# Optimization experiments

Hardware: AMD Instinct MI355X
Metric: run time of the kernel (lower is better)

Reference implementation:

```python
import jax, jax.numpy as jnp
import numpy as np

APP_DIM = 27
FEA_PE = 6
VIEW_PE = 6
FEATURE_C = 128
DENSITY_SHIFT = -10.0
DISTANCE_SCALE = 25.0
IN_MLPC = 2 * VIEW_PE * 3 + 2 * FEA_PE * APP_DIM + 3 + APP_DIM  # 390


def positional_encoding(x, freqs):
    # x: [..., C] -> [..., 2*freqs*C]
    freq_bands = (2.0 ** jnp.arange(freqs)).astype(x.dtype)
    pts = (x[..., None] * freq_bands).reshape(x.shape[:-1] + (freqs * x.shape[-1],))
    return jnp.concatenate([jnp.sin(pts), jnp.cos(pts)], axis=-1)


def alpha2weights(alpha):
    # alpha: [N_rays, N_samples]; last sample forced opaque (as in source)
    alpha = alpha.at[:, -1].set(1.0)
    trans = jnp.concatenate(
        [jnp.ones((alpha.shape[0], 1), alpha.dtype), 1.0 - alpha + 1e-10], axis=-1)
    T = jnp.cumprod(trans, axis=-1)
    weights = alpha * T[:, :-1]
    return weights, T


def setup_inputs() -> dict:
    key = jax.random.key(0)
    ks = jax.random.split(key, 12)
    N_rays, N_samples = 4096, 128
    sigma_feat = jax.random.normal(ks[0], (N_rays, N_samples), jnp.float32)
    app_features = 0.1 * jax.random.normal(ks[1], (N_rays, N_samples, APP_DIM), jnp.float32)
    vd = jax.random.normal(ks[2], (N_rays, N_samples, 3), jnp.float32)
    viewdirs = vd / (jnp.linalg.norm(vd, axis=-1, keepdims=True) + 1e-8)
    dists = 0.02 * jax.random.uniform(ks[3], (N_rays, N_samples), jnp.float32)

    def linear(k, fan_in, fan_out):
        kw, kb = jax.random.split(k)
        lim = 1.0 / np.sqrt(fan_in)
        W = jax.random.uniform(kw, (fan_in, fan_out), jnp.float32, -lim, lim)
        b = jax.random.uniform(kb, (fan_out,), jnp.float32, -lim, lim)
        return W, b

    W1, b1 = linear(ks[4], IN_MLPC, FEATURE_C)
    W2, b2 = linear(ks[5], FEATURE_C, FEATURE_C)
    W3, _ = linear(ks[6], FEATURE_C, 3)
    b3 = jnp.zeros((3,), jnp.float32)  # bias of last layer initialized to 0 in source
    return {"sigma_feat": sigma_feat, "app_features": app_features,
            "viewdirs": viewdirs, "dists": dists,
            "W1": W1, "b1": b1, "W2": W2, "b2": b2, "W3": W3, "b3": b3}


def reference(sigma_feat, app_features, viewdirs, dists, W1, b1, W2, b2, W3, b3):
    # feature2density: softplus with density_shift
    sigma = jax.nn.softplus(sigma_feat + DENSITY_SHIFT)
    alpha = 1.0 - jnp.exp(-sigma * dists * DISTANCE_SCALE)  # [N_rays, N_samples]
    weights, _T = alpha2weights(alpha)

    # MLPRender_Fea: cat[features, viewdirs, PE(features), PE(viewdirs)]
    mlp_in = jnp.concatenate(
        [app_features, viewdirs,
         positional_encoding(app_features, FEA_PE),
         positional_encoding(viewdirs, VIEW_PE)], axis=-1)  # [R, S, 390]
    h = jax.nn.relu(jnp.einsum('rsc,cf->rsf', mlp_in, W1) + b1)
    h = jax.nn.relu(jnp.einsum('rsf,fg->rsg', h, W2) + b2)
    rgb = jax.nn.sigmoid(jnp.einsum('rsg,go->rso', h, W3) + b3)  # [R, S, 3]

    rgb_map = jnp.sum(weights[..., None] * rgb, axis=-2)  # [R, 3]
    return rgb_map
```

## Files before the change

kernel.cpp:

```cpp
#include <hip/hip_runtime.h>
#include <math.h>

typedef unsigned short u16;
using bf16x8 = __attribute__((ext_vector_type(8))) short;
using f32x4  = __attribute__((ext_vector_type(4))) float;

#define NS      128
#define NBLOCKS 4096
#define NSLICE  19

#define POOLSZ 32768
#define OH2    16384

#define BAR() do { asm volatile("s_waitcnt lgkmcnt(0)" ::: "memory");        \
                   __builtin_amdgcn_s_barrier();                              \
                   asm volatile("" ::: "memory"); } while (0)

#define MF(A,B,C) __builtin_amdgcn_mfma_f32_16x16x32_bf16((A),(B),(C),0,0,0)

__device__ __forceinline__ u16 f2bf(float f) {
    unsigned int i = __float_as_uint(f);
    return (u16)((i + 0x7FFFu + ((i >> 16) & 1u)) >> 16);
}

__device__ __forceinline__ unsigned pk(float hi, float lo) {
    unsigned r;
    asm("v_cvt_pk_bf16_f32 %0, %1, %2" : "=v"(r) : "v"(lo), "v"(hi));
    return r;
}
__device__ __forceinline__ u16 f2bf1(float f) {
    return (u16)((__float_as_uint(f) + 0x8000u) >> 16);
}

__device__ __forceinline__ int afoff_h(int m, int k) {
    int chunk = ((k >> 5) * 8 + (m >> 4)) * 64 + ((k >> 3) & 3) * 16 + (m & 15);
    chunk ^= (k >> 3) & 3;
    return chunk * 8 + (k & 7);
}

__device__ __forceinline__ int orig_k(int ch, int slot) {
    if (ch < 27) {
        if (slot == 0) return ch;
        if (slot <= 6) return 30 + ch * 6 + (slot - 1);
        return 192 + ch * 6 + (slot - 7);
    } else {
        int c = ch - 27;
        if (slot == 0) return 27 + c;
        if (slot <= 6) return 354 + c * 6 + (slot - 1);
        return 372 + c * 6 + (slot - 7);
    }
}

__device__ __forceinline__ float ldch(const float* ap, const float* vp, int c) {
    return (c < 27) ? ap[c] : vp[c - 27];
}

__device__ __forceinline__ void build_x(u16* dst, float v) {
    float rev = v * 0.15915494309189535f;
    rev -= floorf(rev);
    float s0 = __builtin_amdgcn_sinf(rev);
    float c0 = __builtin_amdgcn_cosf(rev);
    float s1 = 2.f * s0 * c0, c1 = c0 * c0 - s0 * s0;
    float s2 = 2.f * s1 * c1, c2 = c1 * c1 - s1 * s1;
    float s3 = 2.f * s2 * c2, c3 = c2 * c2 - s2 * s2;
    float s4 = 2.f * s3 * c3, c4 = c3 * c3 - s3 * s3;
    float s5 = 2.f * s4 * c4, c5 = c4 * c4 - s4 * s4;
    uint4 lo, hi;
    lo.x = pk(s0, v);  lo.y = pk(s2, s1);  lo.z = pk(s4, s3);  lo.w = pk(c0, s5);
    hi.x = pk(c2, c1); hi.y = pk(c4, c3);  hi.z = pk(0.f, c5); hi.w = 0u;
    *(uint4*)(dst)       = lo;
    *(uint4*)(dst + 128) = hi;
}

__global__ __launch_bounds__(256) void prep_kernel(
    const float* __restrict__ W1, const float* __restrict__ W2,
    const float* __restrict__ W3, u16* __restrict__ ws)
{
    int idx = blockIdx.x * 256 + threadIdx.x;
    if (idx < 61440) {
        int j = idx & 7, lane = (idx >> 3) & 63, nt = (idx >> 9) & 7, ks = idx >> 12;
        int q = lane >> 4, l15 = lane & 15;
        int klocal = q * 8 + j;
        int ch = ks * 2 + (klocal >> 4);
        int slot = klocal & 15;
        int n = nt * 16 + l15;
        ws[idx] = (slot < 13) ? f2bf(W1[orig_k(ch, slot) * 128 + n]) : (u16)0;
    } else if (idx < 77824) {
        int i2 = idx - 61440;
        int j = i2 & 7, lane = (i2 >> 3) & 63, nt = (i2 >> 9) & 7, ks = i2 >> 12;
        int k = ks * 32 + (lane >> 4) * 8 + j;
        int n = nt * 16 + (lane & 15);
        ws[idx] = f2bf(W2[k * 128 + n]);
    } else if (idx < 79872) {
        int i3 = idx - 77824;
        int j = i3 & 7, lane = (i3 >> 3) & 63, ks = i3 >> 9;
        int k = ks * 32 + (lane >> 4) * 8 + j;
        int n = lane & 15;
        ws[idx] = (n < 3) ? f2bf(W3[k * 3 + n]) : (u16)0;
    }
}

#define LOADB2(N0, N1, s)                                                     \
    if ((s) < NSLICE) {                                                       \
        const u16* wp = wp0 + (s) * 4096;                                     \
        N0 = *(const bf16x8*)(wp);                                            \
        N1 = *(const bf16x8*)(wp + 512);                                      \
    }

#define BODYX(s, C0,C1, N0,N1)                                                \
  {                                                                           \
    LOADB2(N0, N1, (s)+2);                                                    \
    const u16* ab = pool + ((s)&7)*4096 + (wm*256 + lane)*8;                  \
    bf16x8 a0 = *(const bf16x8*)(ab);                                         \
    bf16x8 a1 = *(const bf16x8*)(ab + 512);                                   \
    __builtin_amdgcn_s_setprio(1);                                            \
    acc[0][0]=MF(a0,C0,acc[0][0]); acc[0][1]=MF(a0,C1,acc[0][1]);             \
    acc[1][0]=MF(a1,C0,acc[1][0]); acc[1][1]=MF(a1,C1,acc[1][1]);             \
    a0 = *(const bf16x8*)(ab + 1024);                                         \
    a1 = *(const bf16x8*)(ab + 1536);                                         \
    acc[2][0]=MF(a0,C0,acc[2][0]); acc[2][1]=MF(a0,C1,acc[2][1]);             \
    acc[3][0]=MF(a1,C0,acc[3][0]); acc[3][1]=MF(a1,C1,acc[3][1]);             \
    __builtin_amdgcn_s_setprio(0);                                            \
  }

#define BODYH(s, C0,C1, N0,N1)                                                \
  {                                                                           \
    LOADB2(N0, N1, (s)+2);                                                    \
    int cb = ((((s)-15)*512) + wm*256 + lane) ^ quad;                         \
    bf16x8 a0 = *(const bf16x8*)(pool + cb*8);                                \
    bf16x8 a1 = *(const bf16x8*)(pool + (cb+64)*8);                           \
    __builtin_amdgcn_s_setprio(1);                                            \
    acc[0][0]=MF(a0,C0,acc[0][0]); acc[0][1]=MF(a0,C1,acc[0][1]);             \
    acc[1][0]=MF(a1,C0,acc[1][0]); acc[1][1]=MF(a1,C1,acc[1][1]);             \
    a0 = *(const bf16x8*)(pool + (cb+128)*8);                                 \
    a1 = *(const bf16x8*)(pool + (cb+192)*8);                                 \
    acc[2][0]=MF(a0,C0,acc[2][0]); acc[2][1]=MF(a0,C1,acc[2][1]);             \
    acc[3][0]=MF(a1,C0,acc[3][0]); acc[3][1]=MF(a1,C1,acc[3][1]);             \
    __builtin_amdgcn_s_setprio(0);                                            \
  }

#define GENDQ(p)                                                              \
  {                                                                           \
    if (8*(p)+8  + cl < 30)                                                   \
        build_x(pool + ((2*(p)+2)&3)*8192 + (cl>>1)*4096 + bxoff, pv_a);      \
    if (8*(p)+12 + cl < 30)                                                   \
        build_x(pool + ((2*(p)+3)&3)*8192 + (cl>>1)*4096 + bxoff, pv_b);      \
    pv_a = pv_c; pv_b = pv_d;                                                 \
    if (8*(p)+24 + cl < 30) pv_c = ldch(ap, vp, 8*(p)+24 + cl);               \
    if (8*(p)+28 + cl < 30) pv_d = ldch(ap, vp, 8*(p)+28 + cl);               \
    BAR();                                                                    \
  }

__global__ __launch_bounds__(512, 4) void render_kernel(
    const float* __restrict__ sigma_g, const float* __restrict__ app_g,
    const float* __restrict__ view_g,  const float* __restrict__ dists_g,
    const float* __restrict__ b1_g,    const float* __restrict__ b2_g,
    const float* __restrict__ b3_g,    const u16* __restrict__ ws,
    float* __restrict__ out_g)
{
    __shared__ __align__(16) u16 pool[POOLSZ];
    __shared__ __align__(16) float part[NS * 3];
    __shared__ float scanS;
    __shared__ float sum2[6];

    const int tid  = threadIdx.x;
    const int lane = tid & 63;
    const int wave = tid >> 6;
    const int l15  = lane & 15;
    const int quad = lane >> 4;
    const int wm   = wave >> 2;
    const int wn   = wave & 3;

    const int r  = blockIdx.x;
    const int rb = r * NS;
    const int row = tid & 127;
    const int cl  = tid >> 7;
    const float* ap = app_g  + (rb + row) * 27;
    const float* vp = view_g + (rb + row) * 3;
    const int bxoff = (row >> 4) * 512 + (((cl & 1) * 32) + (row & 15)) * 8;

    const u16* wp0 = ws + (wn * 128 + lane) * 8;
    bf16x8 bP0, bP1, bQ0, bQ1, bR0, bR1;
    LOADB2(bP0, bP1, 0);
    LOADB2(bQ0, bQ1, 1);

    float pv_a = ldch(ap, vp, cl);
    float pv_b = ldch(ap, vp, 4 + cl);
    float pv_c = ldch(ap, vp, 8 + cl);
    float pv_d = ldch(ap, vp, 12 + cl);

    float alpha = 0.f, prod = 1.f, wr = 0.f;
    if (tid < NS) {
        float x  = sigma_g[rb + tid] - 10.f;
        float sp = (x > 20.f) ? x : log1pf(expf(x));
        alpha = 1.f - expf(-sp * dists_g[rb + tid] * 25.f);
        if (tid == NS - 1) alpha = 1.f;
        float tb = 1.f - alpha + 1e-10f;
        prod = tb;
        #pragma unroll
        for (int d = 1; d < 64; d <<= 1) {
            float v = __shfl_up(prod, d);
            if (lane >= d) prod *= v;
        }
        if (tid == 63) scanS = prod;
    }

    build_x(pool +        (cl >> 1) * 4096 + bxoff, pv_a);
    build_x(pool + 8192 + (cl >> 1) * 4096 + bxoff, pv_b);
    pv_a = pv_c; pv_b = pv_d;
    pv_c = ldch(ap, vp, 16 + cl);
    pv_d = ldch(ap, vp, 20 + cl);
    BAR();

    if (tid < NS) {
        float prev = __shfl_up(prod, 1);
        float base = (lane == 0) ? 1.f : prev;
        float scale = (wave == 1) ? scanS : 1.f;
        wr = alpha * base * scale;
    }

    const f32x4 vzero = {0.f, 0.f, 0.f, 0.f};
    f32x4 acc[4][2];
    #pragma unroll
    for (int mt = 0; mt < 4; ++mt)
        #pragma unroll
        for (int nt = 0; nt < 2; ++nt) acc[mt][nt] = vzero;

    BODYX(0,  bP0,bP1, bR0,bR1);
    BODYX(1,  bQ0,bQ1, bP0,bP1);
    BODYX(2,  bR0,bR1, bQ0,bQ1);
    BODYX(3,  bP0,bP1, bR0,bR1);  GENDQ(0);
    BODYX(4,  bQ0,bQ1, bP0,bP1);
    BODYX(5,  bR0,bR1, bQ0,bQ1);
    BODYX(6,  bP0,bP1, bR0,bR1);
    BODYX(7,  bQ0,bQ1, bP0,bP1);  GENDQ(1);
    BODYX(8,  bR0,bR1, bQ0,bQ1);
    BODYX(9,  bP0,bP1, bR0,bR1);
    BODYX(10, bQ0,bQ1, bP0,bP1);
    BODYX(11, bR0,bR1, bQ0,bQ1);  GENDQ(2);
    const float b1r0 = b1_g[wn * 32 + l15];
    const float b1r1 = b1_g[wn * 32 + 16 + l15];
    BODYX(12, bP0,bP1, bR0,bR1);
    BODYX(13, bQ0,bQ1, bP0,bP1);
    BODYX(14, bR0,bR1, bQ0,bQ1);

    #pragma unroll
    for (int mt = 0; mt < 4; ++mt)
        #pragma unroll
        for (int nt = 0; nt < 2; ++nt) {
            int col = wn * 32 + nt * 16 + l15;
            #pragma unroll
            for (int rr = 0; rr < 4; ++rr) {
                int rw = wm * 64 + mt * 16 + quad * 4 + rr;
                pool[afoff_h(rw, col)] =
                    f2bf1(fmaxf(acc[mt][nt][rr] + ((nt == 0) ? b1r0 : b1r1), 0.f));
            }
            acc[mt][nt] = vzero;
        }
    BAR();

    const float b2r0 = b2_g[wn * 32 + l15];
    const float b2r1 = b2_g[wn * 32 + 16 + l15];

    BODYH(15, bP0,bP1, bR0,bR1);
    BODYH(16, bQ0,bQ1, bP0,bP1);
    BODYH(17, bR0,bR1, bQ0,bQ1);
    BODYH(18, bP0,bP1, bR0,bR1);

    #pragma unroll
    for (int mt = 0; mt < 4; ++mt)
        #pragma unroll
        for (int nt = 0; nt < 2; ++nt) {
            int col = wn * 32 + nt * 16 + l15;
            #pragma unroll
            for (int rr = 0; rr < 4; ++rr) {
                int rw = wm * 64 + mt * 16 + quad * 4 + rr;
                pool[OH2 + afoff_h(rw, col)] =
                    f2bf1(fmaxf(acc[mt][nt][rr] + ((nt == 0) ? b2r0 : b2r1), 0.f));
            }
        }
    BAR();

    const u16* w3r = ws + 77824;
    const float b3v = (l15 < 3) ? b3_g[l15] : 0.f;
    f32x4 acc3 = vzero;
    #pragma unroll
    for (int ks = 0; ks < 4; ++ks) {
        bf16x8 w3f = *(const bf16x8*)(w3r + (ks * 64 + lane) * 8);
        int c = ((ks * 8 + wave) * 64 + lane) ^ quad;
        bf16x8 a3 = *(const bf16x8*)(pool + OH2 + c * 8);
        acc3 = MF(a3, w3f, acc3);
    }
    if (l15 < 3) {
        #pragma unroll
        for (int rr = 0; rr < 4; ++rr) {
            int rw = wave * 16 + quad * 4 + rr;
            float v = acc3[rr] + b3v;
            part[rw * 3 + l15] = 1.f / (1.f + expf(-v));
        }
    }
    BAR();

    if (tid < NS) {
        float v0 = wr * part[tid * 3 + 0];
        float v1 = wr * part[tid * 3 + 1];
        float v2 = wr * part[tid * 3 + 2];
        #pragma unroll
        for (int d = 1; d < 64; d <<= 1) {
            v0 += __shfl_xor(v0, d);
            v1 += __shfl_xor(v1, d);
            v2 += __shfl_xor(v2, d);
        }
        if (lane == 0) {
            sum2[wave * 3 + 0] = v0;
            sum2[wave * 3 + 1] = v1;
            sum2[wave * 3 + 2] = v2;
        }
    }
    BAR();
    if (tid == 0) {
        out_g[r * 3 + 0] = sum2[0] + sum2[3];
        out_g[r * 3 + 1] = sum2[1] + sum2[4];
        out_g[r * 3 + 2] = sum2[2] + sum2[5];
    }
}

extern "C" void kernel_launch(void* const* d_in, const int* in_sizes, int n_in,
                              void* d_out, int out_size, void* d_ws, size_t ws_size,
                              hipStream_t stream) {
    (void)in_sizes; (void)n_in; (void)out_size; (void)ws_size;
    const float* sigma = (const float*)d_in[0];
    const float* app   = (const float*)d_in[1];
    const float* view  = (const float*)d_in[2];
    const float* dists = (const float*)d_in[3];
    const float* W1    = (const float*)d_in[4];
    const float* b1    = (const float*)d_in[5];
    const float* W2    = (const float*)d_in[6];
    const float* b2    = (const float*)d_in[7];
    const float* W3    = (const float*)d_in[8];
    const float* b3    = (const float*)d_in[9];
    float* out = (float*)d_out;

    u16* ws = (u16*)d_ws;

    prep_kernel<<<312, 256, 0, stream>>>(W1, W2, W3, ws);
    render_kernel<<<NBLOCKS, 512, 0, stream>>>(sigma, app, view, dists,
                                               b1, b2, b3, ws, out);
}
```

Before: 193.2 us.

## Pack layer-1 K dimension densely by frequency to cut padded MFMA slices

Changes the first-layer K layout from 16 slots per channel (13 used, 3 zero pads) to grouping one frequency term per 32-wide K slice across 30 channels, so layer 1 runs 13 K-slices instead of 15. Each thread now owns 8 channels and produces successive sin/cos terms by repeated angle doubling, writing one slice pair per step into a ring of LDS buffers. The hidden-layer buffers are relocated into the same ring to match. This removes padded MFMA work and reshuffles positional-encoding generation, at the cost of more registers per thread and a different barrier schedule.

Result: no change. 195.1 us (+1.0%).

```diff
diff --git a/kernel.cpp b/kernel.cpp
--- a/kernel.cpp
+++ b/kernel.cpp
@@ -7,10 +7,9 @@
 
 #define NS      128
 #define NBLOCKS 4096
-#define NSLICE  19
+#define NSLICE  17
 
 #define POOLSZ 32768
-#define OH2    16384
 
 #define BAR() do { asm volatile("s_waitcnt lgkmcnt(0)" ::: "memory");        \
                    __builtin_amdgcn_s_barrier();                              \
@@ -32,10 +31,15 @@
     return (u16)((__float_as_uint(f) + 0x8000u) >> 16);
 }
 
-__device__ __forceinline__ int afoff_h(int m, int k) {
-    int chunk = ((k >> 5) * 8 + (m >> 4)) * 64 + ((k >> 3) & 3) * 16 + (m & 15);
-    chunk ^= (k >> 3) & 3;
-    return chunk * 8 + (k & 7);
+__device__ __forceinline__ int afoff_h1(int m, int k) {
+    int e = (k >> 3) & 3;
+    int chunk = (m >> 4) * 64 + e * 16 + (m & 15);
+    return ((5 + (k >> 5)) & 7) * 4096 + (chunk ^ e) * 8 + (k & 7);
+}
+__device__ __forceinline__ int afoff_h2(int m, int k) {
+    int e = (k >> 3) & 3;
+    int chunk = (m >> 4) * 64 + e * 16 + (m & 15);
+    return ((1 + (k >> 5)) & 7) * 4096 + (chunk ^ e) * 8 + (k & 7);
 }
 
 __device__ __forceinline__ int orig_k(int ch, int slot) {
@@ -51,25 +55,9 @@
     }
 }
 
-__device__ __forceinline__ float ldch(const float* ap, const float* vp, int c) {
-    return (c < 27) ? ap[c] : vp[c - 27];
-}
-
-__device__ __forceinline__ void build_x(u16* dst, float v) {
-    float rev = v * 0.15915494309189535f;
-    rev -= floorf(rev);
-    float s0 = __builtin_amdgcn_sinf(rev);
-    float c0 = __builtin_amdgcn_cosf(rev);
-    float s1 = 2.f * s0 * c0, c1 = c0 * c0 - s0 * s0;
-    float s2 = 2.f * s1 * c1, c2 = c1 * c1 - s1 * s1;
-    float s3 = 2.f * s2 * c2, c3 = c2 * c2 - s2 * s2;
-    float s4 = 2.f * s3 * c3, c4 = c3 * c3 - s3 * s3;
-    float s5 = 2.f * s4 * c4, c5 = c4 * c4 - s4 * s4;
-    uint4 lo, hi;
-    lo.x = pk(s0, v);  lo.y = pk(s2, s1);  lo.z = pk(s4, s3);  lo.w = pk(c0, s5);
-    hi.x = pk(c2, c1); hi.y = pk(c4, c3);  hi.z = pk(0.f, c5); hi.w = 0u;
-    *(uint4*)(dst)       = lo;
-    *(uint4*)(dst + 128) = hi;
+__device__ __forceinline__ int cons_slot(int j) {
+    if (j == 0) return 0;
+    return (j & 1) ? (j + 1) / 2 : 6 + j / 2;
 }
 
 __global__ __launch_bounds__(256) void prep_kernel(
@@ -77,24 +65,22 @@
     const float* __restrict__ W3, u16* __restrict__ ws)
 {
     int idx = blockIdx.x * 256 + threadIdx.x;
-    if (idx < 61440) {
-        int j = idx & 7, lane = (idx >> 3) & 63, nt = (idx >> 9) & 7, ks = idx >> 12;
+    if (idx < 53248) {
+        int jj = idx & 7, lane = (idx >> 3) & 63, nt = (idx >> 9) & 7, j = idx >> 12;
         int q = lane >> 4, l15 = lane & 15;
-        int klocal = q * 8 + j;
-        int ch = ks * 2 + (klocal >> 4);
-        int slot = klocal & 15;
+        int ch = q * 8 + jj;
         int n = nt * 16 + l15;
-        ws[idx] = (slot < 13) ? f2bf(W1[orig_k(ch, slot) * 128 + n]) : (u16)0;
-    } else if (idx < 77824) {
-        int i2 = idx - 61440;
-        int j = i2 & 7, lane = (i2 >> 3) & 63, nt = (i2 >> 9) & 7, ks = i2 >> 12;
-        int k = ks * 32 + (lane >> 4) * 8 + j;
+        ws[idx] = (ch < 30) ? f2bf(W1[orig_k(ch, cons_slot(j)) * 128 + n]) : (u16)0;
+    } else if (idx < 69632) {
+        int i2 = idx - 53248;
+        int jj = i2 & 7, lane = (i2 >> 3) & 63, nt = (i2 >> 9) & 7, ks = i2 >> 12;
+        int k = ks * 32 + (lane >> 4) * 8 + jj;
         int n = nt * 16 + (lane & 15);
         ws[idx] = f2bf(W2[k * 128 + n]);
-    } else if (idx < 79872) {
-        int i3 = idx - 77824;
-        int j = i3 & 7, lane = (i3 >> 3) & 63, ks = i3 >> 9;
-        int k = ks * 32 + (lane >> 4) * 8 + j;
+    } else if (idx < 71680) {
+        int i3 = idx - 69632;
+        int jj = i3 & 7, lane = (i3 >> 3) & 63, ks = i3 >> 9;
+        int k = ks * 32 + (lane >> 4) * 8 + jj;
         int n = lane & 15;
         ws[idx] = (n < 3) ? f2bf(W3[k * 3 + n]) : (u16)0;
     }
@@ -126,7 +112,7 @@
 #define BODYH(s, C0,C1, N0,N1)                                                \
   {                                                                           \
     LOADB2(N0, N1, (s)+2);                                                    \
-    int cb = ((((s)-15)*512) + wm*256 + lane) ^ quad;                         \
+    int cb = ((5 + ((s)-13)) & 7) * 512 + ((wm*256 + lane) ^ quad);           \
     bf16x8 a0 = *(const bf16x8*)(pool + cb*8);                                \
     bf16x8 a1 = *(const bf16x8*)(pool + (cb+64)*8);                           \
     __builtin_amdgcn_s_setprio(1);                                            \
@@ -139,17 +125,19 @@
     __builtin_amdgcn_s_setprio(0);                                            \
   }
 
-#define GENDQ(p)                                                              \
-  {                                                                           \
-    if (8*(p)+8  + cl < 30)                                                   \
-        build_x(pool + ((2*(p)+2)&3)*8192 + (cl>>1)*4096 + bxoff, pv_a);      \
-    if (8*(p)+12 + cl < 30)                                                   \
-        build_x(pool + ((2*(p)+3)&3)*8192 + (cl>>1)*4096 + bxoff, pv_b);      \
-    pv_a = pv_c; pv_b = pv_d;                                                 \
-    if (8*(p)+24 + cl < 30) pv_c = ldch(ap, vp, 8*(p)+24 + cl);               \
-    if (8*(p)+28 + cl < 30) pv_d = ldch(ap, vp, 8*(p)+28 + cl);               \
-    BAR();                                                                    \
-  }
+#define W8(j, A)                                                              \
+  { uint4 w_; w_.x = pk(A[1],A[0]); w_.y = pk(A[3],A[2]);                     \
+    w_.z = pk(A[5],A[4]); w_.w = pk(A[7],A[6]);                               \
+    *(uint4*)(pool + ((j)&7)*4096 + bx2) = w_; }
+
+#define DBL(d)                                                                \
+  { _Pragma("unroll")                                                         \
+    for (int i_ = 0; i_ < 8; ++i_) {                                          \
+        float t_ = sreg[i_] * creg[i_];                                       \
+        float u_ = creg[i_] * creg[i_] - sreg[i_] * sreg[i_];                 \
+        sreg[i_] = t_ + t_; creg[i_] = u_;                                    \
+    }                                                                         \
+    W8(1 + 2*(d), sreg); W8(2 + 2*(d), creg); }
 
 __global__ __launch_bounds__(512, 4) void render_kernel(
     const float* __restrict__ sigma_g, const float* __restrict__ app_g,
@@ -174,20 +162,22 @@
     const int r  = blockIdx.x;
     const int rb = r * NS;
     const int row = tid & 127;
-    const int cl  = tid >> 7;
+    const int g   = tid >> 7;
     const float* ap = app_g  + (rb + row) * 27;
     const float* vp = view_g + (rb + row) * 3;
-    const int bxoff = (row >> 4) * 512 + (((cl & 1) * 32) + (row & 15)) * 8;
+    const int bx2 = ((row >> 4) * 64 + g * 16 + (row & 15)) * 8;
 
     const u16* wp0 = ws + (wn * 128 + lane) * 8;
     bf16x8 bP0, bP1, bQ0, bQ1, bR0, bR1;
     LOADB2(bP0, bP1, 0);
     LOADB2(bQ0, bQ1, 1);
 
-    float pv_a = ldch(ap, vp, cl);
-    float pv_b = ldch(ap, vp, 4 + cl);
-    float pv_c = ldch(ap, vp, 8 + cl);
-    float pv_d = ldch(ap, vp, 12 + cl);
+    float v8[8];
+    #pragma unroll
+    for (int i = 0; i < 8; ++i) {
+        int ch = g * 8 + i;
+        v8[i] = (ch < 27) ? ap[ch] : ((ch < 30) ? vp[ch - 27] : 0.f);
+    }
 
     float alpha = 0.f, prod = 1.f, wr = 0.f;
     if (tid < NS) {
@@ -205,11 +195,15 @@
         if (tid == 63) scanS = prod;
     }
 
-    build_x(pool +        (cl >> 1) * 4096 + bxoff, pv_a);
-    build_x(pool + 8192 + (cl >> 1) * 4096 + bxoff, pv_b);
-    pv_a = pv_c; pv_b = pv_d;
-    pv_c = ldch(ap, vp, 16 + cl);
-    pv_d = ldch(ap, vp, 20 + cl);
+    float sreg[8], creg[8];
+    #pragma unroll
+    for (int i = 0; i < 8; ++i) {
+        float rev = v8[i] * 0.15915494309189535f;
+        rev -= floorf(rev);
+        sreg[i] = __builtin_amdgcn_sinf(rev);
+        creg[i] = __builtin_amdgcn_cosf(rev);
+    }
+    W8(0, v8); W8(1, sreg); W8(2, creg);
     BAR();
 
     if (tid < NS) {
@@ -229,20 +223,24 @@
     BODYX(0,  bP0,bP1, bR0,bR1);
     BODYX(1,  bQ0,bQ1, bP0,bP1);
     BODYX(2,  bR0,bR1, bQ0,bQ1);
-    BODYX(3,  bP0,bP1, bR0,bR1);  GENDQ(0);
+    DBL(1); DBL(2);
+    BAR();
+    BODYX(3,  bP0,bP1, bR0,bR1);
     BODYX(4,  bQ0,bQ1, bP0,bP1);
     BODYX(5,  bR0,bR1, bQ0,bQ1);
     BODYX(6,  bP0,bP1, bR0,bR1);
-    BODYX(7,  bQ0,bQ1, bP0,bP1);  GENDQ(1);
+    DBL(3); DBL(4);
+    BAR();
+    BODYX(7,  bQ0,bQ1, bP0,bP1);
     BODYX(8,  bR0,bR1, bQ0,bQ1);
     BODYX(9,  bP0,bP1, bR0,bR1);
     BODYX(10, bQ0,bQ1, bP0,bP1);
-    BODYX(11, bR0,bR1, bQ0,bQ1);  GENDQ(2);
+    DBL(5);
+    BAR();
+    BODYX(11, bR0,bR1, bQ0,bQ1);
     const float b1r0 = b1_g[wn * 32 + l15];
     const float b1r1 = b1_g[wn * 32 + 16 + l15];
     BODYX(12, bP0,bP1, bR0,bR1);
-    BODYX(13, bQ0,bQ1, bP0,bP1);
-    BODYX(14, bR0,bR1, bQ0,bQ1);
 
     #pragma unroll
     for (int mt = 0; mt < 4; ++mt)
@@ -252,7 +250,7 @@
             #pragma unroll
             for (int rr = 0; rr < 4; ++rr) {
                 int rw = wm * 64 + mt * 16 + quad * 4 + rr;
-                pool[afoff_h(rw, col)] =
+                pool[afoff_h1(rw, col)] =
                     f2bf1(fmaxf(acc[mt][nt][rr] + ((nt == 0) ? b1r0 : b1r1), 0.f));
             }
             acc[mt][nt] = vzero;
@@ -262,10 +260,10 @@
     const float b2r0 = b2_g[wn * 32 + l15];
     const float b2r1 = b2_g[wn * 32 + 16 + l15];
 
+    BODYH(13, bQ0,bQ1, bP0,bP1);
+    BODYH(14, bR0,bR1, bQ0,bQ1);
     BODYH(15, bP0,bP1, bR0,bR1);
     BODYH(16, bQ0,bQ1, bP0,bP1);
-    BODYH(17, bR0,bR1, bQ0,bQ1);
-    BODYH(18, bP0,bP1, bR0,bR1);
 
     #pragma unroll
     for (int mt = 0; mt < 4; ++mt)
@@ -275,20 +273,20 @@
             #pragma unroll
             for (int rr = 0; rr < 4; ++rr) {
                 int rw = wm * 64 + mt * 16 + quad * 4 + rr;
-                pool[OH2 + afoff_h(rw, col)] =
+                pool[afoff_h2(rw, col)] =
                     f2bf1(fmaxf(acc[mt][nt][rr] + ((nt == 0) ? b2r0 : b2r1), 0.f));
             }
         }
     BAR();
 
-    const u16* w3r = ws + 77824;
+    const u16* w3r = ws + 69632;
     const float b3v = (l15 < 3) ? b3_g[l15] : 0.f;
     f32x4 acc3 = vzero;
     #pragma unroll
     for (int ks = 0; ks < 4; ++ks) {
         bf16x8 w3f = *(const bf16x8*)(w3r + (ks * 64 + lane) * 8);
-        int c = ((ks * 8 + wave) * 64 + lane) ^ quad;
-        bf16x8 a3 = *(const bf16x8*)(pool + OH2 + c * 8);
+        int c = ((1 + ks) & 7) * 512 + ((wave * 64 + lane) ^ quad);
+        bf16x8 a3 = *(const bf16x8*)(pool + c * 8);
         acc3 = MF(a3, w3f, acc3);
     }
     if (l15 < 3) {
@@ -343,7 +341,7 @@
 
     u16* ws = (u16*)d_ws;
 
-    prep_kernel<<<312, 256, 0, stream>>>(W1, W2, W3, ws);
+    prep_kernel<<<280, 256, 0, stream>>>(W1, W2, W3, ws);
     render_kernel<<<NBLOCKS, 512, 0, stream>>>(sigma, app, view, dists,
                                                b1, b2, b3, ws, out);
 }
```
